# Optimization experiments

Measured on AMD Instinct MI355X. Metric: run time of the kernel, lower is better.

The kernel has to match this reference:

```python
import jax, jax.numpy as jnp
import numpy as np

F = 32          # number of fields
B = 2048        # batch size
K = 64          # embedding dim
H = 64          # attention hidden size
VOCAB = 100000  # hash_size


def setup_inputs() -> dict:
    key = jax.random.key(0)
    ks = jax.random.split(key, 7)
    x = jax.random.randint(ks[0], (F, B), 0, VOCAB)
    emb_v = jax.random.normal(ks[1], (VOCAB, K), jnp.float32) * 0.05
    at_w = jax.random.normal(ks[2], (K, H), jnp.float32) * 0.1
    at_b = jnp.zeros((H,), jnp.float32)
    at_h = jax.random.normal(ks[3], (H, 1), jnp.float32) * 0.1
    p = jax.random.normal(ks[4], (K, 1), jnp.float32) * 0.1
    w0 = jnp.zeros((), jnp.float32)
    w1 = jax.random.normal(ks[5], (VOCAB, 1), jnp.float32) * 0.05
    return {"x": x, "emb_v": emb_v, "at_w": at_w, "at_b": at_b,
            "at_h": at_h, "p": p, "w0": w0, "w1": w1}


def reference(x, emb_v, at_w, at_b, at_h, p, w0, w1):
    # Embedding lookup: [F, B, K]
    V = emb_v[x]
    # Pairwise interactions: all i<j pairs -> [P, B, K], P = F*(F-1)/2
    iu, ju = np.triu_indices(F, k=1)
    VV = V[iu] * V[ju]                                   # [P, B, K]
    # Attention MLP per pair (no softmax in original code)
    hid = jax.nn.relu(jnp.einsum('pbk,kh->pbh', VV, at_w) + at_b)  # [P, B, H]
    score = jnp.einsum('pbh,ho->pbo', hid, at_h)         # [P, B, 1]
    # Attention-weighted sum pooling over pairs -> [B, K]
    pooled = jnp.sum(VV * score, axis=0)
    # Second-order score
    at_fm_score = pooled @ p                             # [B, 1]
    # First-order FM part: sum over fields of w1 lookups
    fm1 = w0 + jnp.sum(w1[x], axis=0)                    # [B, 1]
    logit = at_fm_score + fm1
    prob = jax.nn.sigmoid(logit)
    return prob
```

## Files before the change

kernel.cpp:

```cpp
#include <hip/hip_runtime.h>
#include <math.h>

#define F      32
#define BATCH  2048
#define K      64
#define H      64
#define NPAIR  496
#define NTROW  31

typedef float v4f __attribute__((ext_vector_type(4)));
typedef short v8s __attribute__((ext_vector_type(8)));

__device__ __forceinline__ float bf2f(short s) {
    union { unsigned u; float f; } v;
    v.u = ((unsigned)(unsigned short)s) << 16;
    return v.f;
}
__device__ __forceinline__ short f2bf(float f) {
    union { float f; unsigned u; } v; v.f = f;
    unsigned r = v.u + 0x7fffu + ((v.u >> 16) & 1u);
    return (short)(r >> 16);
}

__global__ __launch_bounds__(256)
void afm_fwd(const int*   __restrict__ x,
             const float* __restrict__ emb_v,
             const float* __restrict__ at_w,
             const float* __restrict__ at_b,
             const float* __restrict__ at_h,
             const float* __restrict__ p,
             const float* __restrict__ w0,
             const float* __restrict__ w1,
             float*       __restrict__ out)
{
    __shared__ __align__(16) short Vsh[F][72];
    __shared__ unsigned char pi_sh[NPAIR], pj_sh[NPAIR];
    __shared__ float fm_sh[F];
    __shared__ float wacc[4];

    const int b    = blockIdx.x;
    const int t    = threadIdx.x;
    const int lane = t & 63;
    const int wv   = t >> 6;
    const int c    = lane & 15;
    const int quad = lane >> 4;

    if (t < F) {
        int i = t;
        int base = i * (2 * F - i - 1) / 2;
        for (int j = i + 1; j < F; ++j) {
            pi_sh[base + (j - i - 1)] = (unsigned char)i;
            pj_sh[base + (j - i - 1)] = (unsigned char)j;
        }
    }

    {
        int f  = t >> 3;
        int cb = (t & 7) * 8;
        int idx = x[f * BATCH + b];
        const float4* src = (const float4*)&emb_v[idx * K + cb];
        float4 a0 = src[0], a1 = src[1];
        v8s w;
        w[0] = f2bf(a0.x); w[1] = f2bf(a0.y); w[2] = f2bf(a0.z); w[3] = f2bf(a0.w);
        w[4] = f2bf(a1.x); w[5] = f2bf(a1.y); w[6] = f2bf(a1.z); w[7] = f2bf(a1.w);
        *(v8s*)&Vsh[f][cb] = w;
    }
    if (t < F) fm_sh[t] = w1[x[t * BATCH + b]];

    v8s bfrag[4][2];
    #pragma unroll
    for (int nt = 0; nt < 4; ++nt)
        #pragma unroll
        for (int kk = 0; kk < 2; ++kk)
            #pragma unroll
            for (int e = 0; e < 8; ++e)
                bfrag[nt][kk][e] = f2bf(at_w[(kk * 32 + quad * 8 + e) * H + nt * 16 + c]);

    float ab[4], ah[4];
    #pragma unroll
    for (int nt = 0; nt < 4; ++nt) {
        ab[nt] = at_b[nt * 16 + c];
        ah[nt] = at_h[nt * 16 + c];
    }
    float preg[16];
    #pragma unroll
    for (int kk = 0; kk < 2; ++kk) {
        float4 p0 = *(const float4*)&p[kk * 32 + quad * 8];
        float4 p1 = *(const float4*)&p[kk * 32 + quad * 8 + 4];
        preg[kk * 8 + 0] = p0.x; preg[kk * 8 + 1] = p0.y;
        preg[kk * 8 + 2] = p0.z; preg[kk * 8 + 3] = p0.w;
        preg[kk * 8 + 4] = p1.x; preg[kk * 8 + 5] = p1.y;
        preg[kk * 8 + 6] = p1.z; preg[kk * 8 + 7] = p1.w;
    }

    __syncthreads();

    float accTot = 0.f;

    for (int tr = wv; tr < NTROW; tr += 4) {
        int pr = tr * 16 + c;
        int pi = pi_sh[pr], pj = pj_sh[pr];

        v8s af[2];
        float qp = 0.f;
        #pragma unroll
        for (int kk = 0; kk < 2; ++kk) {
            v8s vi = *(const v8s*)&Vsh[pi][kk * 32 + quad * 8];
            v8s vj = *(const v8s*)&Vsh[pj][kk * 32 + quad * 8];
            #pragma unroll
            for (int e = 0; e < 8; ++e) {
                float prod = bf2f(vi[e]) * bf2f(vj[e]);
                af[kk][e] = f2bf(prod);
                qp = fmaf(prod, preg[kk * 8 + e], qp);
            }
        }

        v4f acc[4];
        #pragma unroll
        for (int nt = 0; nt < 4; ++nt) {
            acc[nt] = (v4f){0.f, 0.f, 0.f, 0.f};
            #pragma unroll
            for (int kk = 0; kk < 2; ++kk)
                acc[nt] = __builtin_amdgcn_mfma_f32_16x16x32_bf16(af[kk], bfrag[nt][kk], acc[nt], 0, 0, 0);
        }

        float scr[4];
        #pragma unroll
        for (int r = 0; r < 4; ++r) {
            float s = 0.f;
            #pragma unroll
            for (int nt = 0; nt < 4; ++nt) {
                float pre = acc[nt][r] + ab[nt];
                s = fmaf(fmaxf(pre, 0.f), ah[nt], s);
            }
            s += __shfl_xor(s, 1);
            s += __shfl_xor(s, 2);
            s += __shfl_xor(s, 4);
            s += __shfl_xor(s, 8);
            scr[r] = s;
        }
        qp += __shfl_xor(qp, 16);
        qp += __shfl_xor(qp, 32);

        float sSel = (c & 2) ? ((c & 1) ? scr[3] : scr[2])
                             : ((c & 1) ? scr[1] : scr[0]);
        if ((c >> 2) == quad) accTot = fmaf(sSel, qp, accTot);
    }

    accTot += __shfl_xor(accTot, 1);
    accTot += __shfl_xor(accTot, 2);
    accTot += __shfl_xor(accTot, 4);
    accTot += __shfl_xor(accTot, 8);
    accTot += __shfl_xor(accTot, 16);
    accTot += __shfl_xor(accTot, 32);
    if (lane == 0) wacc[wv] = accTot;
    __syncthreads();

    if (t == 0) {
        float fm1 = w0[0];
        #pragma unroll
        for (int f = 0; f < F; ++f) fm1 += fm_sh[f];
        float logit = wacc[0] + wacc[1] + wacc[2] + wacc[3] + fm1;
        out[b] = 1.f / (1.f + expf(-logit));
    }
}

extern "C" void kernel_launch(void* const* d_in, const int* in_sizes, int n_in,
                              void* d_out, int out_size, void* d_ws, size_t ws_size,
                              hipStream_t stream) {
    const int*   x     = (const int*)  d_in[0];
    const float* emb_v = (const float*)d_in[1];
    const float* at_w  = (const float*)d_in[2];
    const float* at_b  = (const float*)d_in[3];
    const float* at_h  = (const float*)d_in[4];
    const float* p     = (const float*)d_in[5];
    const float* w0    = (const float*)d_in[6];
    const float* w1    = (const float*)d_in[7];
    float* out = (float*)d_out;

    afm_fwd<<<BATCH, 256, 0, stream>>>(x, emb_v, at_w, at_b, at_h, p, w0, w1, out);
}
```

Measured before the change: 109.6 us.

## Precompute bf16 weight fragments and pair table; fold p projection into MFMA

A small setup kernel converts at_w to bf16 MFMA B-fragments, adds p as a fifth N-tile, and builds a packed (i,j) pair table in workspace. The main kernel now loads these fragments as vectors instead of doing per-element strided loads and conversions in every block. Computing VV·p with the MFMA lets each lane multiply its partial hidden score by the projection directly, which removes the per-row shuffle reductions and the lane-select logic. In exchange there is an extra kernel launch per call and p is applied in bf16 rather than fp32.

```diff
diff --git a/kernel.cpp b/kernel.cpp
--- a/kernel.cpp
+++ b/kernel.cpp
@@ -7,6 +7,9 @@
 #define H      64
 #define NPAIR  496
 #define NTROW  31
+
+#define WS_BFRAG_SHORTS (5 * 2 * 64 * 8)
+#define WS_PAIRS_OFF    10240
 
 typedef float v4f __attribute__((ext_vector_type(4)));
 typedef short v8s __attribute__((ext_vector_type(8)));
@@ -22,19 +25,54 @@
     return (short)(r >> 16);
 }
 
+__global__ void afm_setup(const float* __restrict__ at_w,
+                          const float* __restrict__ p,
+                          short* __restrict__ bfrag_ws,
+                          int*   __restrict__ pairs_ws)
+{
+    int idx = blockIdx.x * blockDim.x + threadIdx.x;
+
+    if (idx < 5 * 2 * 64) {
+        int nt   = idx >> 7;
+        int rem  = idx & 127;
+        int kk   = rem >> 6;
+        int lane = rem & 63;
+        int quad = lane >> 4, c = lane & 15;
+        v8s w;
+        #pragma unroll
+        for (int e = 0; e < 8; ++e) {
+            int k = kk * 32 + quad * 8 + e;
+            float val = (nt < 4) ? at_w[k * H + nt * 16 + c] : p[k];
+            w[e] = f2bf(val);
+        }
+        *(v8s*)&bfrag_ws[idx * 8] = w;
+    }
+
+    if (idx < NTROW * 16) {
+        int tr = idx >> 4, c = idx & 15;
+        int pr = tr * 16 + c;
+        int i = 0, rem = pr;
+        while (rem >= F - 1 - i) { rem -= F - 1 - i; ++i; }
+        int j = i + 1 + rem;
+        int packed = i | (j << 8);
+        #pragma unroll
+        for (int q = 0; q < 4; ++q)
+            pairs_ws[tr * 64 + q * 16 + c] = packed;
+    }
+}
+
 __global__ __launch_bounds__(256)
 void afm_fwd(const int*   __restrict__ x,
              const float* __restrict__ emb_v,
-             const float* __restrict__ at_w,
              const float* __restrict__ at_b,
              const float* __restrict__ at_h,
-             const float* __restrict__ p,
              const float* __restrict__ w0,
              const float* __restrict__ w1,
+             const short* __restrict__ bfrag_ws,
+             const int*   __restrict__ pairs_ws,
              float*       __restrict__ out)
 {
     __shared__ __align__(16) short Vsh[F][72];
-    __shared__ unsigned char pi_sh[NPAIR], pj_sh[NPAIR];
     __shared__ float fm_sh[F];
     __shared__ float wacc[4];
 
@@ -44,15 +82,6 @@
     const int wv   = t >> 6;
     const int c    = lane & 15;
     const int quad = lane >> 4;
-
-    if (t < F) {
-        int i = t;
-        int base = i * (2 * F - i - 1) / 2;
-        for (int j = i + 1; j < F; ++j) {
-            pi_sh[base + (j - i - 1)] = (unsigned char)i;
-            pj_sh[base + (j - i - 1)] = (unsigned char)j;
-        }
-    }
 
     {
         int f  = t >> 3;
@@ -67,14 +96,12 @@
     }
     if (t < F) fm_sh[t] = w1[x[t * BATCH + b]];
 
-    v8s bfrag[4][2];
+    v8s bf[5][2];
     #pragma unroll
-    for (int nt = 0; nt < 4; ++nt)
+    for (int nt = 0; nt < 5; ++nt)
         #pragma unroll
         for (int kk = 0; kk < 2; ++kk)
-            #pragma unroll
-            for (int e = 0; e < 8; ++e)
-                bfrag[nt][kk][e] = f2bf(at_w[(kk * 32 + quad * 8 + e) * H + nt * 16 + c]);
+            bf[nt][kk] = *(const v8s*)&bfrag_ws[((nt * 2 + kk) * 64 + lane) * 8];
 
     float ab[4], ah[4];
     #pragma unroll
@@ -82,69 +109,51 @@
         ab[nt] = at_b[nt * 16 + c];
         ah[nt] = at_h[nt * 16 + c];
     }
-    float preg[16];
+
+    int prk[8];
     #pragma unroll
-    for (int kk = 0; kk < 2; ++kk) {
-        float4 p0 = *(const float4*)&p[kk * 32 + quad * 8];
-        float4 p1 = *(const float4*)&p[kk * 32 + quad * 8 + 4];
-        preg[kk * 8 + 0] = p0.x; preg[kk * 8 + 1] = p0.y;
-        preg[kk * 8 + 2] = p0.z; preg[kk * 8 + 3] = p0.w;
-        preg[kk * 8 + 4] = p1.x; preg[kk * 8 + 5] = p1.y;
-        preg[kk * 8 + 6] = p1.z; preg[kk * 8 + 7] = p1.w;
+    for (int s = 0; s < 8; ++s) {
+        int tr = wv + 4 * s;
+        prk[s] = (tr < NTROW) ? pairs_ws[tr * 64 + lane] : 0;
     }
 
     __syncthreads();
 
     float accTot = 0.f;
 
-    for (int tr = wv; tr < NTROW; tr += 4) {
-        int pr = tr * 16 + c;
-        int pi = pi_sh[pr], pj = pj_sh[pr];
+    #pragma unroll
+    for (int s = 0; s < 8; ++s) {
+        int tr = wv + 4 * s;
+        if (tr >= NTROW) break;
+        int pi = prk[s] & 255, pj = (prk[s] >> 8) & 255;
 
         v8s af[2];
-        float qp = 0.f;
         #pragma unroll
         for (int kk = 0; kk < 2; ++kk) {
             v8s vi = *(const v8s*)&Vsh[pi][kk * 32 + quad * 8];
             v8s vj = *(const v8s*)&Vsh[pj][kk * 32 + quad * 8];
             #pragma unroll
-            for (int e = 0; e < 8; ++e) {
-                float prod = bf2f(vi[e]) * bf2f(vj[e]);
-                af[kk][e] = f2bf(prod);
-                qp = fmaf(prod, preg[kk * 8 + e], qp);
-            }
+            for (int e = 0; e < 8; ++e)
+                af[kk][e] = f2bf(bf2f(vi[e]) * bf2f(vj[e]));
         }
 
-        v4f acc[4];
+        v4f acc[5];
         #pragma unroll
-        for (int nt = 0; nt < 4; ++nt) {
+        for (int nt = 0; nt < 5; ++nt) {
             acc[nt] = (v4f){0.f, 0.f, 0.f, 0.f};
             #pragma unroll
             for (int kk = 0; kk < 2; ++kk)
-                acc[nt] = __builtin_amdgcn_mfma_f32_16x16x32_bf16(af[kk], bfrag[nt][kk], acc[nt], 0, 0, 0);
+                acc[nt] = __builtin_amdgcn_mfma_f32_16x16x32_bf16(af[kk], bf[nt][kk], acc[nt], 0, 0, 0);
         }
 
-        float scr[4];
         #pragma unroll
         for (int r = 0; r < 4; ++r) {
-            float s = 0.f;
+            float sp = 0.f;
             #pragma unroll
-            for (int nt = 0; nt < 4; ++nt) {
-                float pre = acc[nt][r] + ab[nt];
-                s = fmaf(fmaxf(pre, 0.f), ah[nt], s);
-            }
-            s += __shfl_xor(s, 1);
-            s += __shfl_xor(s, 2);
-            s += __shfl_xor(s, 4);
-            s += __shfl_xor(s, 8);
-            scr[r] = s;
+            for (int nt = 0; nt < 4; ++nt)
+                sp = fmaf(fmaxf(acc[nt][r] + ab[nt], 0.f), ah[nt], sp);
+            accTot = fmaf(acc[4][r], sp, accTot);
         }
-        qp += __shfl_xor(qp, 16);
-        qp += __shfl_xor(qp, 32);
-
-        float sSel = (c & 2) ? ((c & 1) ? scr[3] : scr[2])
-                             : ((c & 1) ? scr[1] : scr[0]);
-        if ((c >> 2) == quad) accTot = fmaf(sSel, qp, accTot);
     }
 
     accTot += __shfl_xor(accTot, 1);
@@ -178,5 +187,10 @@
     const float* w1    = (const float*)d_in[7];
     float* out = (float*)d_out;
 
-    afm_fwd<<<BATCH, 256, 0, stream>>>(x, emb_v, at_w, at_b, at_h, p, w0, w1, out);
+    short* bfrag_ws = (short*)d_ws;
+    int*   pairs_ws = (int*)((char*)d_ws + WS_PAIRS_OFF);
+
+    afm_setup<<<3, 256, 0, stream>>>(at_w, p, bfrag_ws, pairs_ws);
+    afm_fwd<<<BATCH, 256, 0, stream>>>(x, emb_v, at_b, at_h, w0, w1,
+                                       bfrag_ws, pairs_ws, out);
 }
```

Result: no change. 108.1 us (-1.4%).
